# Kernel optimization log

Hardware: AMD Instinct MI355X
Metric: run time of the kernel (lower is better)

## Reference

```python
import jax, jax.numpy as jnp
import numpy as np

N_NODES = 50000
N_EDGES = 800000
NFEAT, NHID, NCLASS = 512, 128, 40


def spmm(row, col, w, x, n):
    # sparse adj (COO) @ dense x : gather source rows, scale, segment-sum into dest
    return jax.ops.segment_sum(w[:, None] * x[col], row, num_segments=n)


def setup_inputs() -> dict:
    key = jax.random.key(0)
    ks = jax.random.split(key, 8)
    x = jax.random.normal(ks[0], (N_NODES, NFEAT), dtype=jnp.float32)
    edge_row = jax.random.randint(ks[1], (N_EDGES,), 0, N_NODES, dtype=jnp.int32)
    edge_col = jax.random.randint(ks[2], (N_EDGES,), 0, N_NODES, dtype=jnp.int32)
    edge_weight = jax.random.uniform(ks[3], (N_EDGES,), dtype=jnp.float32)
    # Glorot-style init as in GraphConvolution.reset_parameters
    w1 = jax.random.normal(ks[4], (NFEAT, NHID), dtype=jnp.float32) / np.sqrt(NFEAT)
    b1 = jax.random.normal(ks[5], (NHID,), dtype=jnp.float32) * 0.01
    w2 = jax.random.normal(ks[6], (NHID, NCLASS), dtype=jnp.float32) / np.sqrt(NHID)
    b2 = jax.random.normal(ks[7], (NCLASS,), dtype=jnp.float32) * 0.01
    return {"x": x, "edge_row": edge_row, "edge_col": edge_col,
            "edge_weight": edge_weight, "w1": w1, "b1": b1, "w2": w2, "b2": b2}


def reference(x, edge_row, edge_col, edge_weight, w1, b1, w2, b2):
    n = x.shape[0]
    # layer 1: relu(adj @ (x @ w1) + b1)   (dropout is identity in eval mode)
    h = jax.nn.relu(spmm(edge_row, edge_col, edge_weight, x @ w1, n) + b1)
    # layer 2: adj @ (h @ w2) + b2
    out = spmm(edge_row, edge_col, edge_weight, h @ w2, n) + b2
    return out
```

## Files before the change

### kernel.cpp

```cpp
#include <hip/hip_runtime.h>
#include <hip/hip_bf16.h>
#include <cstddef>


typedef float f32x4 __attribute__((ext_vector_type(4)));
typedef short bf16x8 __attribute__((ext_vector_type(8)));

static __device__ __forceinline__ short f2bf(float f) {
    __hip_bfloat16 b = __float2bfloat16(f);
    return *reinterpret_cast<short*>(&b);
}
static __device__ __forceinline__ float bflo(unsigned u) {
    union { unsigned i; float f; } v; v.i = u << 16; return v.f;
}
static __device__ __forceinline__ float bfhi(unsigned u) {
    union { unsigned i; float f; } v; v.i = u & 0xFFFF0000u; return v.f;
}
static __device__ __forceinline__ unsigned pack2bf(float lo, float hi) {
    unsigned a = (unsigned short)f2bf(lo);
    unsigned b = (unsigned short)f2bf(hi);
    return a | (b << 16);
}

typedef const __attribute__((address_space(1))) void* gas_ptr;
typedef __attribute__((address_space(3))) void* las_ptr;
static __device__ __forceinline__ void gload16(const void* g, void* l) {
    __builtin_amdgcn_global_load_lds((gas_ptr)g, (las_ptr)l, 16, 0, 0);
}

__global__ __launch_bounds__(256) void prep_kernel(
    const float* __restrict__ W1, short* __restrict__ W1Tb,
    const float* __restrict__ W2, short* __restrict__ W2Ts,
    int* __restrict__ cur, int N)
{
    int idx = blockIdx.x * 256 + threadIdx.x;
    if (idx < 65536) {
        int k = idx >> 7, n = idx & 127;
        W1Tb[n * 512 + k] = f2bf(W1[idx]);
    } else if (idx < 65536 + 6144) {
        int i2 = idx - 65536;
        int n = i2 >> 7, k = i2 & 127;
        W2Ts[i2 ^ ((n & 7) << 3)] = (n < 40) ? f2bf(W2[k * 40 + n]) : (short)0;
    } else if (idx < 65536 + 6144 + N) {
        cur[idx - 65536 - 6144] = 0;
    }
}

__global__ __launch_bounds__(256) void hist_kernel(const int* __restrict__ row,
                                                   int* __restrict__ counts, int E)
{
    int e = blockIdx.x * 256 + threadIdx.x;
    if (e < E) atomicAdd(&counts[row[e]], 1);
}

__global__ __launch_bounds__(256) void scan1_kernel(const int* __restrict__ counts,
                                                    int* __restrict__ excl,
                                                    int* __restrict__ bsum, int N)
{
    __shared__ int s[256];
    const int t = threadIdx.x;
    const int i = blockIdx.x * 256 + t;
    int v = (i < N) ? counts[i] : 0;
    s[t] = v; __syncthreads();
#pragma unroll
    for (int off = 1; off < 256; off <<= 1) {
        int tmp = (t >= off) ? s[t - off] : 0;
        __syncthreads();
        s[t] += tmp;
        __syncthreads();
    }
    if (i < N) excl[i] = s[t] - v;
    if (t == 255) bsum[blockIdx.x] = s[255];
}

__global__ __launch_bounds__(256) void scan23_kernel(int* __restrict__ rowptr,
                                                     const int* __restrict__ bsum,
                                                     int* __restrict__ cur,
                                                     int N, int E, int NB)
{
    __shared__ int s[256];
    const int t = threadIdx.x;
    int v = (t < NB) ? bsum[t] : 0;
    s[t] = v; __syncthreads();
#pragma unroll
    for (int off = 1; off < 256; off <<= 1) {
        int tmp = (t >= off) ? s[t - off] : 0;
        __syncthreads();
        s[t] += tmp;
        __syncthreads();
    }
    const int add = (blockIdx.x > 0) ? s[blockIdx.x - 1] : 0;
    const int i = blockIdx.x * 256 + t;
    if (i < N) {
        int v2 = rowptr[i] + add;
        rowptr[i] = v2;
        cur[i] = v2;
    }
    if (i == 0) rowptr[N] = E;
}

__global__ __launch_bounds__(256, 6) void gemm1_sort_kernel(
    const float* __restrict__ X, const short* __restrict__ W1Tb,
    short* __restrict__ XW1b, int M, int G1,
    const int* __restrict__ erow, const int* __restrict__ ecol,
    const float* __restrict__ ew, int* __restrict__ cur,
    int2* __restrict__ se, int E)
{
    __shared__ __align__(16) short As[64 * 40];
    __shared__ __align__(16) short Bs[128 * 40];

    const int tid = threadIdx.x;

    if (blockIdx.x >= G1) {
        int e = (blockIdx.x - G1) * 256 + tid;
        if (e < E) {
            int r = erow[e];
            int pos = atomicAdd(&cur[r], 1);
            se[pos] = make_int2(ecol[e], __float_as_int(ew[e]));
        }
        return;
    }

    const int w   = tid >> 6;
    const int l   = tid & 63;
    const int l15 = l & 15;
    const int l4  = l >> 4;
    const int row0 = blockIdx.x * 64;
    const int rb   = (w & 1) * 32;
    const int cb   = (w >> 1) * 64;

    const int sr = tid >> 2;
    const int sc = (tid & 3) * 8;
    const int ga = row0 + sr < M ? row0 + sr : M - 1;
    const float* ax = X + (size_t)ga * 512 + sc;
    const int bn = tid >> 1;
    const int bk = (tid & 1) * 16;
    const short* bw = W1Tb + (size_t)bn * 512 + bk;

    f32x4 acc[2][4];
#pragma unroll
    for (int i = 0; i < 2; ++i)
#pragma unroll
        for (int f = 0; f < 4; ++f) acc[i][f] = (f32x4)0.f;

    float4 a0 = *(const float4*)(ax);
    float4 a1 = *(const float4*)(ax + 4);
    bf16x8 bv0 = *(const bf16x8*)(bw);
    bf16x8 bv1 = *(const bf16x8*)(bw + 8);

#pragma unroll
    for (int kt = 0; kt < 16; ++kt) {
        __syncthreads();
        bf16x8 av;
        av[0]=f2bf(a0.x); av[1]=f2bf(a0.y); av[2]=f2bf(a0.z); av[3]=f2bf(a0.w);
        av[4]=f2bf(a1.x); av[5]=f2bf(a1.y); av[6]=f2bf(a1.z); av[7]=f2bf(a1.w);
        *(bf16x8*)&As[sr * 40 + sc] = av;
        *(bf16x8*)&Bs[bn * 40 + bk] = bv0;
        *(bf16x8*)&Bs[bn * 40 + bk + 8] = bv1;
        __syncthreads();

        if (kt < 15) {
            a0 = *(const float4*)(ax + (kt + 1) * 32);
            a1 = *(const float4*)(ax + (kt + 1) * 32 + 4);
            bv0 = *(const bf16x8*)(bw + (kt + 1) * 32);
            bv1 = *(const bf16x8*)(bw + (kt + 1) * 32 + 8);
        }

        bf16x8 af0 = *(const bf16x8*)&As[(rb + l15) * 40 + l4 * 8];
        bf16x8 af1 = *(const bf16x8*)&As[(rb + 16 + l15) * 40 + l4 * 8];
#pragma unroll
        for (int f = 0; f < 4; ++f) {
            const bf16x8 bf_ = *(const bf16x8*)&Bs[(cb + f * 16 + l15) * 40 + l4 * 8];
            acc[0][f] = __builtin_amdgcn_mfma_f32_16x16x32_bf16(af0, bf_, acc[0][f], 0, 0, 0);
            acc[1][f] = __builtin_amdgcn_mfma_f32_16x16x32_bf16(af1, bf_, acc[1][f], 0, 0, 0);
        }
    }

#pragma unroll
    for (int i = 0; i < 2; ++i)
#pragma unroll
        for (int r = 0; r < 4; ++r) {
            const int row = row0 + rb + i * 16 + l4 * 4 + r;
            if (row < M) {
#pragma unroll
                for (int f = 0; f < 4; ++f)
                    XW1b[(size_t)row * 128 + cb + f * 16 + l15] = f2bf(acc[i][f][r]);
            }
        }
}

__global__ __launch_bounds__(256) void seg1g2_kernel(
    const int* __restrict__ rowptr, const int2* __restrict__ se,
    const uint4* __restrict__ x4, const float* __restrict__ b1,
    const short* __restrict__ W2Ts, unsigned short* __restrict__ h48, int N)
{
    __shared__ __align__(16) short Ws[48 * 128];
    __shared__ __align__(16) short Hs[16 * 136];

    const int tid  = threadIdx.x;
    const int w    = tid >> 6;
    const int lane = tid & 63;
    const int qt   = lane >> 4;
    const int ql   = lane & 15;
    const int row0q = blockIdx.x * 4;
    const int r  = row0q + w;
    const int rc = r < N ? r : N - 1;

    {
        const char* src = (const char*)W2Ts;
        char* dst = (char*)Ws;
#pragma unroll
        for (int i = 0; i < 3; ++i)
            gload16(src + i * 4096 + tid * 16, dst + i * 4096 + tid * 16);
    }

    float acc[8];
    if (qt == 0) {
        const float4 ba = *(const float4*)(b1 + 8 * ql);
        const float4 bb = *(const float4*)(b1 + 8 * ql + 4);
        acc[0]=ba.x; acc[1]=ba.y; acc[2]=ba.z; acc[3]=ba.w;
        acc[4]=bb.x; acc[5]=bb.y; acc[6]=bb.z; acc[7]=bb.w;
    } else {
#pragma unroll
        for (int i = 0; i < 8; ++i) acc[i] = 0.f;
    }

    int j = rowptr[rc];
    const int end = rowptr[rc + 1];
    for (; j + 7 < end; j += 8) {
        const int2 ea = se[j + qt];
        const int2 eb = se[j + 4 + qt];
        const uint4 ua = x4[(size_t)ea.x * 16 + ql];
        const uint4 ub = x4[(size_t)eb.x * 16 + ql];
        const float wa = __int_as_float(ea.y), wb = __int_as_float(eb.y);
        acc[0] = fmaf(wa, bflo(ua.x), acc[0]); acc[1] = fmaf(wa, bfhi(ua.x), acc[1]);
        acc[2] = fmaf(wa, bflo(ua.y), acc[2]); acc[3] = fmaf(wa, bfhi(ua.y), acc[3]);
        acc[4] = fmaf(wa, bflo(ua.z), acc[4]); acc[5] = fmaf(wa, bfhi(ua.z), acc[5]);
        acc[6] = fmaf(wa, bflo(ua.w), acc[6]); acc[7] = fmaf(wa, bfhi(ua.w), acc[7]);
        acc[0] = fmaf(wb, bflo(ub.x), acc[0]); acc[1] = fmaf(wb, bfhi(ub.x), acc[1]);
        acc[2] = fmaf(wb, bflo(ub.y), acc[2]); acc[3] = fmaf(wb, bfhi(ub.y), acc[3]);
        acc[4] = fmaf(wb, bflo(ub.z), acc[4]); acc[5] = fmaf(wb, bfhi(ub.z), acc[5]);
        acc[6] = fmaf(wb, bflo(ub.w), acc[6]); acc[7] = fmaf(wb, bfhi(ub.w), acc[7]);
    }
    for (; j < end; j += 4) {
        const int idx = j + qt;
        const int ic  = idx < end ? idx : end - 1;
        const int2 e  = se[ic];
        const float wt = idx < end ? __int_as_float(e.y) : 0.f;
        const uint4 u = x4[(size_t)e.x * 16 + ql];
        acc[0] = fmaf(wt, bflo(u.x), acc[0]); acc[1] = fmaf(wt, bfhi(u.x), acc[1]);
        acc[2] = fmaf(wt, bflo(u.y), acc[2]); acc[3] = fmaf(wt, bfhi(u.y), acc[3]);
        acc[4] = fmaf(wt, bflo(u.z), acc[4]); acc[5] = fmaf(wt, bfhi(u.z), acc[5]);
        acc[6] = fmaf(wt, bflo(u.w), acc[6]); acc[7] = fmaf(wt, bfhi(u.w), acc[7]);
    }
#pragma unroll
    for (int i = 0; i < 8; ++i) {
        acc[i] += __shfl_xor(acc[i], 16);
        acc[i] += __shfl_xor(acc[i], 32);
    }
    if (qt == 0) {
        uint4 o;
        o.x = pack2bf(fmaxf(acc[0], 0.f), fmaxf(acc[1], 0.f));
        o.y = pack2bf(fmaxf(acc[2], 0.f), fmaxf(acc[3], 0.f));
        o.z = pack2bf(fmaxf(acc[4], 0.f), fmaxf(acc[5], 0.f));
        o.w = pack2bf(fmaxf(acc[6], 0.f), fmaxf(acc[7], 0.f));
        *(uint4*)&Hs[w * 136 + ql * 8] = o;
    }
    __syncthreads();

    if (tid < 64) {
        const int l15 = lane & 15;
        const int l4  = lane >> 4;
        const int swz = (l15 & 7) << 3;
        f32x4 acc2[3];
#pragma unroll
        for (int f = 0; f < 3; ++f) acc2[f] = (f32x4)0.f;
#pragma unroll
        for (int kt = 0; kt < 4; ++kt) {
            const bf16x8 a = *(const bf16x8*)&Hs[l15 * 136 + kt * 32 + l4 * 8];
#pragma unroll
            for (int f = 0; f < 3; ++f) {
                const int si = ((f * 16 + l15) * 128 + kt * 32 + l4 * 8) ^ swz;
                const bf16x8 b = *(const bf16x8*)&Ws[si];
                acc2[f] = __builtin_amdgcn_mfma_f32_16x16x32_bf16(a, b, acc2[f], 0, 0, 0);
            }
        }
        if (l4 == 0) {
#pragma unroll
            for (int rr = 0; rr < 4; ++rr) {
                const int grow = row0q + rr;
                if (grow < N) {
#pragma unroll
                    for (int f = 0; f < 3; ++f)
                        h48[(size_t)grow * 48 + f * 16 + l15] =
                            (unsigned short)f2bf(acc2[f][rr]);
                }
            }
        }
    }
}

__global__ __launch_bounds__(256) void segment2_kernel(
    const int* __restrict__ rowptr, const int2* __restrict__ se,
    const uint2* __restrict__ h48, const float* __restrict__ b2,
    float* __restrict__ out, int N)
{
    const int w    = threadIdx.x >> 6;
    const int lane = threadIdx.x & 63;
    const int qt   = lane >> 4;
    const int ql   = lane & 15;
    const int r = blockIdx.x * 4 + w;
    if (r >= N) return;

    float acc[4];
    if (qt == 0 && ql < 10) {
        const float4 bb = *(const float4*)(b2 + 4 * ql);
        acc[0]=bb.x; acc[1]=bb.y; acc[2]=bb.z; acc[3]=bb.w;
    } else {
#pragma unroll
        for (int i = 0; i < 4; ++i) acc[i] = 0.f;
    }

    int j = rowptr[r];
    const int end = rowptr[r + 1];
    for (; j + 7 < end; j += 8) {
        const int2 ea = se[j + qt];
        const int2 eb = se[j + 4 + qt];
        const uint2 ua = h48[(size_t)ea.x * 12 + ql];
        const uint2 ub = h48[(size_t)eb.x * 12 + ql];
        const float wa = __int_as_float(ea.y), wb = __int_as_float(eb.y);
        acc[0] = fmaf(wa, bflo(ua.x), acc[0]); acc[1] = fmaf(wa, bfhi(ua.x), acc[1]);
        acc[2] = fmaf(wa, bflo(ua.y), acc[2]); acc[3] = fmaf(wa, bfhi(ua.y), acc[3]);
        acc[0] = fmaf(wb, bflo(ub.x), acc[0]); acc[1] = fmaf(wb, bfhi(ub.x), acc[1]);
        acc[2] = fmaf(wb, bflo(ub.y), acc[2]); acc[3] = fmaf(wb, bfhi(ub.y), acc[3]);
    }
    for (; j < end; j += 4) {
        const int idx = j + qt;
        const int ic  = idx < end ? idx : end - 1;
        const int2 e  = se[ic];
        const float wt = idx < end ? __int_as_float(e.y) : 0.f;
        const uint2 u = h48[(size_t)e.x * 12 + ql];
        acc[0] = fmaf(wt, bflo(u.x), acc[0]); acc[1] = fmaf(wt, bfhi(u.x), acc[1]);
        acc[2] = fmaf(wt, bflo(u.y), acc[2]); acc[3] = fmaf(wt, bfhi(u.y), acc[3]);
    }
#pragma unroll
    for (int i = 0; i < 4; ++i) {
        acc[i] += __shfl_xor(acc[i], 16);
        acc[i] += __shfl_xor(acc[i], 32);
    }
    if (qt == 0 && ql < 10) {
        float4 o; o.x = acc[0]; o.y = acc[1]; o.z = acc[2]; o.w = acc[3];
        *(float4*)(out + (size_t)r * 40 + 4 * ql) = o;
    }
}

extern "C" void kernel_launch(void* const* d_in, const int* in_sizes, int n_in,
                              void* d_out, int out_size, void* d_ws, size_t ws_size,
                              hipStream_t stream)
{
    const float* x  = (const float*)d_in[0];
    const int* erow = (const int*)d_in[1];
    const int* ecol = (const int*)d_in[2];
    const float* ew = (const float*)d_in[3];
    const float* w1 = (const float*)d_in[4];
    const float* b1 = (const float*)d_in[5];
    const float* w2 = (const float*)d_in[6];
    const float* b2 = (const float*)d_in[7];
    float* out = (float*)d_out;

    const int N = in_sizes[0] / 512;
    const int E = in_sizes[1];
    const int NB = (N + 255) / 256;

    short* w1tb = (short*)d_ws;
    short* w2ts = w1tb + 65536;
    short* xw1b = w2ts + 8192;
    short* h48  = xw1b + (size_t)N * 128;
    int* rowptr = (int*)(h48 + (size_t)N * 128);
    int* cur    = rowptr + (N + 1);
    int* bsum   = cur + N;
    int2* se    = (int2*)(bsum + 256 + ((N + 1) & 1));

    prep_kernel<<<(65536 + 6144 + N + 255) / 256, 256, 0, stream>>>(w1, w1tb, w2, w2ts, cur, N);
    hist_kernel<<<(E + 255) / 256, 256, 0, stream>>>(erow, cur, E);
    scan1_kernel<<<NB, 256, 0, stream>>>(cur, rowptr, bsum, N);
    scan23_kernel<<<NB, 256, 0, stream>>>(rowptr, bsum, cur, N, E, NB);

    const int G1 = (N + 63) / 64;
    const int GS = (E + 255) / 256;
    gemm1_sort_kernel<<<G1 + GS, 256, 0, stream>>>(x, w1tb, xw1b, N, G1,
                                                   erow, ecol, ew, cur, se, E);

    seg1g2_kernel<<<(N + 3) / 4, 256, 0, stream>>>(rowptr, se,
                                                   (const uint4*)xw1b, b1,
                                                   w2ts, (unsigned short*)h48, N);

    segment2_kernel<<<(N + 3) / 4, 256, 0, stream>>>(rowptr, se,
                                                     (const uint2*)h48, b2, out, N);
}
```

Before: 155.4 us.

## Double-buffer LDS and prefetch three K-tiles ahead in gemm1

```diff
diff --git a/kernel.cpp b/kernel.cpp
--- a/kernel.cpp
+++ b/kernel.cpp
@@ -20,6 +20,9 @@
     unsigned a = (unsigned short)f2bf(lo);
     unsigned b = (unsigned short)f2bf(hi);
     return a | (b << 16);
+}
+static __device__ __forceinline__ uint2 cvt4(float4 v) {
+    return make_uint2(pack2bf(v.x, v.y), pack2bf(v.z, v.w));
 }
 
 typedef const __attribute__((address_space(1))) void* gas_ptr;
@@ -99,15 +102,15 @@
     if (i == 0) rowptr[N] = E;
 }
 
-__global__ __launch_bounds__(256, 6) void gemm1_sort_kernel(
+__global__ __launch_bounds__(256, 5) void gemm1_sort_kernel(
     const float* __restrict__ X, const short* __restrict__ W1Tb,
     short* __restrict__ XW1b, int M, int G1,
     const int* __restrict__ erow, const int* __restrict__ ecol,
     const float* __restrict__ ew, int* __restrict__ cur,
     int2* __restrict__ se, int E)
 {
-    __shared__ __align__(16) short As[64 * 40];
-    __shared__ __align__(16) short Bs[128 * 40];
+    __shared__ __align__(16) short As[2][64 * 40];
+    __shared__ __align__(16) short Bs[2][128 * 40];
 
     const int tid = threadIdx.x;
 
@@ -129,13 +132,16 @@
     const int rb   = (w & 1) * 32;
     const int cb   = (w >> 1) * 64;
 
-    const int sr = tid >> 2;
-    const int sc = (tid & 3) * 8;
-    const int ga = row0 + sr < M ? row0 + sr : M - 1;
-    const float* ax = X + (size_t)ga * 512 + sc;
-    const int bn = tid >> 1;
-    const int bk = (tid & 1) * 16;
-    const short* bw = W1Tb + (size_t)bn * 512 + bk;
+    const int arow = tid >> 3;
+    const int acol = (tid & 7) * 4;
+    const int ar0 = row0 + arow,      ac0 = ar0 < M ? ar0 : M - 1;
+    const int ar1 = row0 + 32 + arow, ac1 = ar1 < M ? ar1 : M - 1;
+    const float* ap0 = X + (size_t)ac0 * 512 + acol;
+    const float* ap1 = X + (size_t)ac1 * 512 + acol;
+    const int brow = tid >> 2;
+    const int bcol = (tid & 3) * 8;
+    const short* bp0 = W1Tb + (size_t)brow * 512 + bcol;
+    const short* bp1 = W1Tb + (size_t)(64 + brow) * 512 + bcol;
 
     f32x4 acc[2][4];
 #pragma unroll
@@ -143,38 +149,50 @@
 #pragma unroll
         for (int f = 0; f < 4; ++f) acc[i][f] = (f32x4)0.f;
 
-    float4 a0 = *(const float4*)(ax);
-    float4 a1 = *(const float4*)(ax + 4);
-    bf16x8 bv0 = *(const bf16x8*)(bw);
-    bf16x8 bv1 = *(const bf16x8*)(bw + 8);
+    float4 pa[3][2];
+    bf16x8 pb[3][2];
+
+#define LOADSET(s, kt)                                              \
+    do {                                                            \
+        pa[s][0] = *(const float4*)(ap0 + (kt) * 32);               \
+        pa[s][1] = *(const float4*)(ap1 + (kt) * 32);               \
+        pb[s][0] = *(const bf16x8*)(bp0 + (kt) * 32);               \
+        pb[s][1] = *(const bf16x8*)(bp1 + (kt) * 32);               \
+    } while (0)
+
+#define WRITESET(buf, s)                                            \
+    do {                                                            \
+        *(uint2*)&As[buf][arow * 40 + acol]        = cvt4(pa[s][0]);\
+        *(uint2*)&As[buf][(32 + arow) * 40 + acol] = cvt4(pa[s][1]);\
+        *(bf16x8*)&Bs[buf][brow * 40 + bcol]       = pb[s][0];      \
+        *(bf16x8*)&Bs[buf][(64 + brow) * 40 + bcol] = pb[s][1];     \
+    } while (0)
+
+    LOADSET(0, 0);
+    LOADSET(1, 1);
+    LOADSET(2, 2);
+    WRITESET(0, 0);
+    __syncthreads();
 
 #pragma unroll
     for (int kt = 0; kt < 16; ++kt) {
+        if (kt + 1 < 16) WRITESET((kt + 1) & 1, (kt + 1) % 3);
+        if (kt + 3 < 16) LOADSET(kt % 3, kt + 3);
+        {
+            const int b = kt & 1;
+            bf16x8 af0 = *(const bf16x8*)&As[b][(rb + l15) * 40 + l4 * 8];
+            bf16x8 af1 = *(const bf16x8*)&As[b][(rb + 16 + l15) * 40 + l4 * 8];
+#pragma unroll
+            for (int f = 0; f < 4; ++f) {
+                const bf16x8 bf_ = *(const bf16x8*)&Bs[b][(cb + f * 16 + l15) * 40 + l4 * 8];
+                acc[0][f] = __builtin_amdgcn_mfma_f32_16x16x32_bf16(af0, bf_, acc[0][f], 0, 0, 0);
+                acc[1][f] = __builtin_amdgcn_mfma_f32_16x16x32_bf16(af1, bf_, acc[1][f], 0, 0, 0);
+            }
+        }
         __syncthreads();
-        bf16x8 av;
-        av[0]=f2bf(a0.x); av[1]=f2bf(a0.y); av[2]=f2bf(a0.z); av[3]=f2bf(a0.w);
-        av[4]=f2bf(a1.x); av[5]=f2bf(a1.y); av[6]=f2bf(a1.z); av[7]=f2bf(a1.w);
-        *(bf16x8*)&As[sr * 40 + sc] = av;
-        *(bf16x8*)&Bs[bn * 40 + bk] = bv0;
-        *(bf16x8*)&Bs[bn * 40 + bk + 8] = bv1;
-        __syncthreads();
-
-        if (kt < 15) {
-            a0 = *(const float4*)(ax + (kt + 1) * 32);
-            a1 = *(const float4*)(ax + (kt + 1) * 32 + 4);
-            bv0 = *(const bf16x8*)(bw + (kt + 1) * 32);
-            bv1 = *(const bf16x8*)(bw + (kt + 1) * 32 + 8);
-        }
-
-        bf16x8 af0 = *(const bf16x8*)&As[(rb + l15) * 40 + l4 * 8];
-        bf16x8 af1 = *(const bf16x8*)&As[(rb + 16 + l15) * 40 + l4 * 8];
-#pragma unroll
-        for (int f = 0; f < 4; ++f) {
-            const bf16x8 bf_ = *(const bf16x8*)&Bs[(cb + f * 16 + l15) * 40 + l4 * 8];
-            acc[0][f] = __builtin_amdgcn_mfma_f32_16x16x32_bf16(af0, bf_, acc[0][f], 0, 0, 0);
-            acc[1][f] = __builtin_amdgcn_mfma_f32_16x16x32_bf16(af1, bf_, acc[1][f], 0, 0, 0);
-        }
-    }
+    }
+#undef LOADSET
+#undef WRITESET
 
 #pragma unroll
     for (int i = 0; i < 2; ++i)
```

Measured after the change: 163.1 us. +5.0%, slower.
